# Performance work log

Hardware: AMD Instinct MI355X
Metric: run time of the kernel (lower is better)

## Reference

```python
import jax, jax.numpy as jnp
import numpy as np

B, S, DIM = 4, 2048, 1024


def _xavier(key, shape):
    # xavier_uniform for a [out, in] Linear weight
    fan_in, fan_out = shape[1], shape[0]
    limit = float(np.sqrt(6.0 / (fan_in + fan_out)))
    return jax.random.uniform(key, shape, jnp.float32, -limit, limit)


def setup_inputs() -> dict:
    key = jax.random.key(0)
    ks = jax.random.split(key, 8)
    z_real = jax.random.normal(ks[0], (B, S, DIM), jnp.float32)
    z_imag = jax.random.normal(ks[1], (B, S, DIM), jnp.float32)
    wq_r = _xavier(ks[2], (DIM, DIM))
    wq_i = _xavier(ks[3], (DIM, DIM))
    wk_r = _xavier(ks[4], (DIM, DIM))
    wk_i = _xavier(ks[5], (DIM, DIM))
    wv_r = _xavier(ks[6], (DIM, DIM))
    wv_i = _xavier(ks[7], (DIM, DIM))
    # causal mask (0 = masked), broadcast over batch
    mask = jnp.tril(jnp.ones((S, S), jnp.int32))
    return {"z_real": z_real, "z_imag": z_imag,
            "wq_r": wq_r, "wq_i": wq_i,
            "wk_r": wk_r, "wk_i": wk_i,
            "wv_r": wv_r, "wv_i": wv_i,
            "mask": mask}


def _complex_linear(xr, xi, wr, wi):
    # torch Linear: y = x @ W^T
    yr = xr @ wr.T - xi @ wi.T
    yi = xi @ wr.T + xr @ wi.T
    return yr, yi


def reference(z_real, z_imag, wq_r, wq_i, wk_r, wk_i, wv_r, wv_i, mask):
    dim = z_real.shape[-1]
    scale = dim ** (-0.5)
    qr, qi = _complex_linear(z_real, z_imag, wq_r, wq_i)
    kr, ki = _complex_linear(z_real, z_imag, wk_r, wk_i)
    vr, vi = _complex_linear(z_real, z_imag, wv_r, wv_i)
    # cat([q.real, q.imag]) @ cat([k.real, k.imag])^T == qr@kr^T + qi@ki^T
    scores = (jnp.einsum('bsd,btd->bst', qr, kr)
              + jnp.einsum('bsd,btd->bst', qi, ki)) * scale  # [B,S,S]
    scores = jnp.where(mask == 0, -jnp.inf, scores)
    attn = jax.nn.softmax(scores, axis=-1)
    out_r = jnp.einsum('bst,btd->bsd', attn, vr)
    out_i = jnp.einsum('bst,btd->bsd', attn, vi)
    return jnp.stack([out_r, out_i], axis=0)  # [2,B,S,dim] = (real, imag)
```

## Files before the change

kernel.cpp:

```cpp
#include <hip/hip_runtime.h>
#include <hip/hip_bf16.h>
#include <hip/hip_fp16.h>

#define DIMK 1024
#define SEQ  2048
#define BATCH 4
#define NTOK (BATCH*SEQ)
#define PROJ_ELEMS ((size_t)NTOK*DIMK)
#define LD 2048

typedef unsigned short ushort_t;
typedef __attribute__((ext_vector_type(8))) short short8;
typedef __attribute__((ext_vector_type(4))) float float4v;

#define MFMA_BF16 __builtin_amdgcn_mfma_f32_16x16x32_bf16

__device__ __forceinline__ unsigned short f2bf(float f) {
    union { float f; unsigned int i; } x; x.f = f;
    unsigned int r = x.i + 0x7fffu + ((x.i >> 16) & 1u);
    return (unsigned short)(r >> 16);
}

__device__ __forceinline__ void gld_lds16(const void* g, void* l) {
    auto gp = reinterpret_cast<const __attribute__((address_space(1))) unsigned int*>(
        reinterpret_cast<uintptr_t>(g));
    auto lp = reinterpret_cast<__attribute__((address_space(3))) unsigned int*>(
        reinterpret_cast<uintptr_t>(l));
    __builtin_amdgcn_global_load_lds(gp, lp, 16, 0, 0);
}

__device__ __forceinline__ void stage2(const ushort_t* __restrict__ gbase,
                                       ushort_t* lbase, int kcol,
                                       int rg0, int g, int scol)
{
    gld_lds16(gbase + (size_t)(rg0 * 16 + g) * LD + kcol + scol,
              lbase + rg0 * 512);
    gld_lds16(gbase + (size_t)(rg0 * 16 + 16 + g) * LD + kcol + scol,
              lbase + rg0 * 512 + 512);
}

__device__ __forceinline__ void gemm_core256(
    const ushort_t* __restrict__ Arow,
    const ushort_t* __restrict__ Brow,
    int kend,
    ushort_t* Alds, ushort_t* Blds,
    float4v acc[8][4], int wid, int lane)
{
    const int g    = lane >> 2;
    const int sx   = lane & 3;
    const int scol = ((sx - (g >> 1)) & 3) * 8;
    const int r16  = lane & 15;
    const int quad = lane >> 4;
    const int roff = r16 * 32 + ((quad + (r16 >> 1)) & 3) * 8;
    const int wm = wid >> 2, wn = wid & 3;
    const int rg0 = wid * 2;
    const int NT = kend >> 6;

    stage2(Brow, Blds,        0,  rg0, g, scol);
    stage2(Arow, Alds,        0,  rg0, g, scol);
    stage2(Brow, Blds + 8192, 32, rg0, g, scol);
    stage2(Arow, Alds + 8192, 32, rg0, g, scol);
    asm volatile("s_waitcnt vmcnt(4)" ::: "memory");
    __builtin_amdgcn_s_barrier();

    for (int t = 0; t < NT; ++t) {
        const int d     = (t & 1) << 14;
        const int dn    = d ^ 16384;
        const int knext = (t + 1) << 6;
        const bool pre  = (t + 1 < NT);
        short8 af[4], bf[4];

        #pragma unroll
        for (int j = 0; j < 4; ++j)
            bf[j] = *(const short8*)(Blds + d + (wn * 4 + j) * 512 + roff);
        #pragma unroll
        for (int ii = 0; ii < 4; ++ii)
            af[ii] = *(const short8*)(Alds + d + (wm * 8 + ii) * 512 + roff);
        if (pre) stage2(Brow, Blds + dn, knext, rg0, g, scol);
        asm volatile("" ::: "memory");
        __builtin_amdgcn_s_barrier();
        asm volatile("s_waitcnt lgkmcnt(0)" ::: "memory");
        __builtin_amdgcn_s_setprio(1);
        #pragma unroll
        for (int ii = 0; ii < 4; ++ii)
            #pragma unroll
            for (int j = 0; j < 4; ++j)
                acc[ii][j] = MFMA_BF16(af[ii], bf[j], acc[ii][j], 0, 0, 0);
        __builtin_amdgcn_s_setprio(0);
        asm volatile("" ::: "memory");
        __builtin_amdgcn_s_barrier();

        #pragma unroll
        for (int ii = 0; ii < 4; ++ii)
            af[ii] = *(const short8*)(Alds + d + (wm * 8 + 4 + ii) * 512 + roff);
        if (pre) {
            stage2(Arow, Alds + dn, knext, rg0, g, scol);
            asm volatile("s_waitcnt vmcnt(4)" ::: "memory");
        } else {
            asm volatile("s_waitcnt vmcnt(0)" ::: "memory");
        }
        __builtin_amdgcn_s_barrier();
        asm volatile("s_waitcnt lgkmcnt(0)" ::: "memory");
        __builtin_amdgcn_s_setprio(1);
        #pragma unroll
        for (int ii = 0; ii < 4; ++ii)
            #pragma unroll
            for (int j = 0; j < 4; ++j)
                acc[4 + ii][j] = MFMA_BF16(af[ii], bf[j], acc[4 + ii][j], 0, 0, 0);
        __builtin_amdgcn_s_setprio(0);
        asm volatile("" ::: "memory");
        __builtin_amdgcn_s_barrier();

        #pragma unroll
        for (int j = 0; j < 4; ++j)
            bf[j] = *(const short8*)(Blds + d + 8192 + (wn * 4 + j) * 512 + roff);
        #pragma unroll
        for (int ii = 0; ii < 4; ++ii)
            af[ii] = *(const short8*)(Alds + d + 8192 + (wm * 8 + ii) * 512 + roff);
        if (pre) stage2(Brow, Blds + dn + 8192, knext + 32, rg0, g, scol);
        asm volatile("" ::: "memory");
        __builtin_amdgcn_s_barrier();
        asm volatile("s_waitcnt lgkmcnt(0)" ::: "memory");
        __builtin_amdgcn_s_setprio(1);
        #pragma unroll
        for (int ii = 0; ii < 4; ++ii)
            #pragma unroll
            for (int j = 0; j < 4; ++j)
                acc[ii][j] = MFMA_BF16(af[ii], bf[j], acc[ii][j], 0, 0, 0);
        __builtin_amdgcn_s_setprio(0);
        asm volatile("" ::: "memory");
        __builtin_amdgcn_s_barrier();

        #pragma unroll
        for (int ii = 0; ii < 4; ++ii)
            af[ii] = *(const short8*)(Alds + d + 8192 + (wm * 8 + 4 + ii) * 512 + roff);
        if (pre) {
            stage2(Arow, Alds + dn + 8192, knext + 32, rg0, g, scol);
            asm volatile("s_waitcnt vmcnt(4)" ::: "memory");
        } else {
            asm volatile("" ::: "memory");
        }
        __builtin_amdgcn_s_barrier();
        asm volatile("s_waitcnt lgkmcnt(0)" ::: "memory");
        __builtin_amdgcn_s_setprio(1);
        #pragma unroll
        for (int ii = 0; ii < 4; ++ii)
            #pragma unroll
            for (int j = 0; j < 4; ++j)
                acc[4 + ii][j] = MFMA_BF16(af[ii], bf[j], acc[4 + ii][j], 0, 0, 0);
        __builtin_amdgcn_s_setprio(0);
        asm volatile("" ::: "memory");
        __builtin_amdgcn_s_barrier();
    }
}

__global__ __launch_bounds__(512, 2)
void gemm_proj(const ushort_t* __restrict__ A, const ushort_t* __restrict__ B,
               ushort_t* __restrict__ Cq, ushort_t* __restrict__ Ck,
               ushort_t* __restrict__ Cv)
{
    __shared__ ushort_t smem[65536];
    const int tid = threadIdx.x, wid = tid >> 6, lane = tid & 63;
    const int m0 = blockIdx.y * 256;
    const int n0g = blockIdx.x * 256;
    ushort_t* C = (n0g < 2048) ? Cq : ((n0g < 4096) ? Ck : Cv);
    const int n0 = n0g & 2047;
    float4v acc[8][4] = {};
    gemm_core256(A + (size_t)m0 * LD, B + (size_t)n0g * LD, 2048,
                 smem, smem + 32768, acc, wid, lane);

    const int wm = wid >> 2, wn = wid & 3;
    const int col16 = lane & 15, quad = lane >> 4;
    #pragma unroll
    for (int i = 0; i < 8; ++i)
        #pragma unroll
        for (int j = 0; j < 4; ++j) {
            const int n = n0 + wn * 64 + j * 16 + col16;
            #pragma unroll
            for (int r = 0; r < 4; ++r) {
                const int m = m0 + wm * 128 + i * 16 + quad * 4 + r;
                C[(size_t)m * LD + n] = f2bf(acc[i][j][r]);
            }
        }
}

__global__ __launch_bounds__(512, 2)
void gemm_scores(const ushort_t* __restrict__ Q, const ushort_t* __restrict__ K,
                 __half* __restrict__ S)
{
    const int jt = blockIdx.x, it = blockIdx.y, b = blockIdx.z;
    if (jt > it) return;
    __shared__ ushort_t smem[65536];
    const int tid = threadIdx.x, wid = tid >> 6, lane = tid & 63;
    const size_t boff = (size_t)b * SEQ * LD;
    float4v acc[8][4] = {};
    gemm_core256(Q + boff + (size_t)it * 256 * LD, K + boff + (size_t)jt * 256 * LD,
                 2048, smem, smem + 32768, acc, wid, lane);

    const int wm = wid >> 2, wn = wid & 3;
    const int col16 = lane & 15, quad = lane >> 4;
    const float scale = 0.03125f;
    __half* Sb = S + (size_t)b * SEQ * SEQ;
    #pragma unroll
    for (int i = 0; i < 8; ++i)
        #pragma unroll
        for (int j = 0; j < 4; ++j) {
            const int t = jt * 256 + wn * 64 + j * 16 + col16;
            #pragma unroll
            for (int r = 0; r < 4; ++r) {
                const int s = it * 256 + wm * 128 + i * 16 + quad * 4 + r;
                Sb[(size_t)s * SEQ + t] = __float2half(acc[i][j][r] * scale);
            }
        }
}

__global__ __launch_bounds__(512, 2)
void gemm_pv(const ushort_t* __restrict__ P, const ushort_t* __restrict__ VT,
             float* __restrict__ out)
{
    const int nt = blockIdx.x, mt = blockIdx.y, b = blockIdx.z;
    __shared__ ushort_t smem[65536];
    const int tid = threadIdx.x, wid = tid >> 6, lane = tid & 63;
    const int kend = (mt + 1) * 256;
    float4v acc[8][4] = {};
    gemm_core256(P + (size_t)b * SEQ * SEQ + (size_t)mt * 256 * LD,
                 VT + (size_t)b * LD * LD + (size_t)nt * 256 * LD,
                 kend, smem, smem + 32768, acc, wid, lane);

    const int wm = wid >> 2, wn = wid & 3;
    const int col16 = lane & 15, quad = lane >> 4;
    #pragma unroll
    for (int i = 0; i < 8; ++i)
        #pragma unroll
        for (int j = 0; j < 4; ++j) {
            const int n = nt * 256 + wn * 64 + j * 16 + col16;
            float* dst = out + ((n < 1024) ? 0 : PROJ_ELEMS);
            const int d = n & 1023;
            #pragma unroll
            for (int r = 0; r < 4; ++r) {
                const int s = mt * 256 + wm * 128 + i * 16 + quad * 4 + r;
                dst[((size_t)b * SEQ + s) * DIMK + d] = acc[i][j][r];
            }
        }
}

__global__ __launch_bounds__(256)
void zcat_kernel(const float* __restrict__ zr, const float* __restrict__ zi,
                 ushort_t* __restrict__ zcat)
{
    const size_t e = ((size_t)blockIdx.x * 256 + threadIdx.x) * 8;
    const size_t tok = e >> 11;
    const int c = (int)(e & 2047);
    const float* src = (c < 1024) ? (zr + tok * 1024 + c) : (zi + tok * 1024 + (c - 1024));
    float4 a = *(const float4*)src;
    float4 b = *(const float4*)(src + 4);
    ushort_t* d = zcat + e;
    d[0]=f2bf(a.x); d[1]=f2bf(a.y); d[2]=f2bf(a.z); d[3]=f2bf(a.w);
    d[4]=f2bf(b.x); d[5]=f2bf(b.y); d[6]=f2bf(b.z); d[7]=f2bf(b.w);
}

__global__ __launch_bounds__(256)
void wstack_kernel(const float* __restrict__ wr, const float* __restrict__ wi,
                   ushort_t* __restrict__ ws)
{
    const size_t e = ((size_t)blockIdx.x * 256 + threadIdx.x) * 8;
    const int n = (int)(e >> 11), c = (int)(e & 2047);
    const int n1 = n & 1023, c1 = c & 1023;
    const float* src;
    float sgn = 1.f;
    if (n < 1024) {
        if (c < 1024) src = wr + (size_t)n1 * 1024 + c1;
        else        { src = wi + (size_t)n1 * 1024 + c1; sgn = -1.f; }
    } else {
        src = ((c < 1024) ? wi : wr) + (size_t)n1 * 1024 + c1;
    }
    float4 a = *(const float4*)src;
    float4 b = *(const float4*)(src + 4);
    ushort_t* d = ws + e;
    d[0]=f2bf(sgn*a.x); d[1]=f2bf(sgn*a.y); d[2]=f2bf(sgn*a.z); d[3]=f2bf(sgn*a.w);
    d[4]=f2bf(sgn*b.x); d[5]=f2bf(sgn*b.y); d[6]=f2bf(sgn*b.z); d[7]=f2bf(sgn*b.w);
}

__global__ __launch_bounds__(256)
void transpose_v(const ushort_t* __restrict__ vcat, ushort_t* __restrict__ vt)
{
    __shared__ ushort_t tile[64][65];
    const int b = blockIdx.z;
    const int t0 = blockIdx.x * 64, c0 = blockIdx.y * 64;
    const int tid = threadIdx.x;
    const int r = tid >> 4, c4 = (tid & 15) * 4;
    const ushort_t* src = vcat + ((size_t)(b * SEQ + t0)) * LD + c0;
    #pragma unroll
    for (int p = 0; p < 4; ++p) {
        const int row = p * 16 + r;
        ushort4 v = *(const ushort4*)(src + (size_t)row * LD + c4);
        tile[row][c4+0]=v.x; tile[row][c4+1]=v.y; tile[row][c4+2]=v.z; tile[row][c4+3]=v.w;
    }
    __syncthreads();
    ushort_t* dst = vt + ((size_t)b * LD + c0) * LD + t0;
    #pragma unroll
    for (int p = 0; p < 4; ++p) {
        const int crow = p * 16 + r;
        ushort4 v;
        v.x = tile[c4+0][crow]; v.y = tile[c4+1][crow];
        v.z = tile[c4+2][crow]; v.w = tile[c4+3][crow];
        *(ushort4*)(dst + (size_t)crow * LD + c4) = v;
    }
}

__global__ __launch_bounds__(256)
void softmax_kernel(__half* __restrict__ sc)
{
    const int row = blockIdx.x;
    const int s = row & (SEQ - 1);
    __half* x = sc + (size_t)row * SEQ;
    ushort_t* xo = (ushort_t*)x;
    const int n = s + 1;
    const int tid = threadIdx.x, wave = tid >> 6, lane = tid & 63;
    __shared__ float redm[4], reds[4];

    float m = -1e30f;
    for (int i = tid; i < n; i += 256) m = fmaxf(m, __half2float(x[i]));
    #pragma unroll
    for (int off = 32; off > 0; off >>= 1) m = fmaxf(m, __shfl_down(m, off, 64));
    if (lane == 0) redm[wave] = m;
    __syncthreads();
    if (tid == 0) redm[0] = fmaxf(fmaxf(redm[0], redm[1]), fmaxf(redm[2], redm[3]));
    __syncthreads();
    m = redm[0];

    float l = 0.f;
    for (int i = tid; i < n; i += 256) l += __expf(__half2float(x[i]) - m);
    #pragma unroll
    for (int off = 32; off > 0; off >>= 1) l += __shfl_down(l, off, 64);
    if (lane == 0) reds[wave] = l;
    __syncthreads();
    if (tid == 0) reds[0] = reds[0] + reds[1] + reds[2] + reds[3];
    __syncthreads();
    const float inv = 1.0f / reds[0];

    const int npad = min(SEQ, ((s >> 8) + 1) << 8);
    for (int i = tid; i < npad; i += 256) {
        float v = (i < n) ? __expf(__half2float(x[i]) - m) * inv : 0.f;
        xo[i] = f2bf(v);
    }
}

extern "C" void kernel_launch(void* const* d_in, const int* in_sizes, int n_in,
                              void* d_out, int out_size, void* d_ws, size_t ws_size,
                              hipStream_t stream)
{
    const float* z_real = (const float*)d_in[0];
    const float* z_imag = (const float*)d_in[1];
    const float* wq_r   = (const float*)d_in[2];
    const float* wq_i   = (const float*)d_in[3];
    const float* wk_r   = (const float*)d_in[4];
    const float* wk_i   = (const float*)d_in[5];
    const float* wv_r   = (const float*)d_in[6];
    const float* wv_i   = (const float*)d_in[7];

    uint8_t* ws = (uint8_t*)d_ws;
    ushort_t* zcat = (ushort_t*)(ws + 0);
    ushort_t* wall = (ushort_t*)(ws + 33554432);
    ushort_t* wsq  = wall;
    ushort_t* wsk  = (ushort_t*)(ws + 33554432 + 8388608);
    ushort_t* wsv  = (ushort_t*)(ws + 33554432 + 16777216);
    ushort_t* qcat = (ushort_t*)(ws + 58720256);
    ushort_t* kcat = (ushort_t*)(ws + 92274688);
    ushort_t* vcat = (ushort_t*)(ws + 125829120);
    ushort_t* vt   = (ushort_t*)(ws + 0);
    __half*   sc   = (__half*)(ws + 125829120);
    float*    outp = (float*)d_out;

    zcat_kernel<<<dim3(8192), dim3(256), 0, stream>>>(z_real, z_imag, zcat);
    wstack_kernel<<<dim3(2048), dim3(256), 0, stream>>>(wq_r, wq_i, wsq);
    wstack_kernel<<<dim3(2048), dim3(256), 0, stream>>>(wk_r, wk_i, wsk);
    wstack_kernel<<<dim3(2048), dim3(256), 0, stream>>>(wv_r, wv_i, wsv);

    gemm_proj<<<dim3(24, 32), dim3(512), 0, stream>>>(zcat, wall, qcat, kcat, vcat);

    transpose_v<<<dim3(32, 32, 4), dim3(256), 0, stream>>>(vcat, vt);
    gemm_scores<<<dim3(8, 8, 4), dim3(512), 0, stream>>>(qcat, kcat, sc);
    softmax_kernel<<<dim3(NTOK), dim3(256), 0, stream>>>(sc);
    gemm_pv<<<dim3(8, 8, 4), dim3(512), 0, stream>>>((ushort_t*)sc, vt, outp);
}
```

Before: 491.3 us.

## Double-buffer MFMA register fragments to overlap LDS reads with compute

Restructures the GEMM main loop so each phase reads the next fragment set from LDS into a second register buffer while MFMAs run on the previously loaded one. The explicit lgkmcnt(0) waits before each MFMA block are removed. Global-to-LDS staging of A and B is now issued together, with the vmcnt waits moved after compute. This hides LDS latency behind matrix math at the cost of more live VGPRs. It also risks subtle ordering hazards around the shared buffers.

```diff
diff --git a/kernel.cpp b/kernel.cpp
--- a/kernel.cpp
+++ b/kernel.cpp
@@ -52,9 +52,12 @@
     const int r16  = lane & 15;
     const int quad = lane >> 4;
     const int roff = r16 * 32 + ((quad + (r16 >> 1)) & 3) * 8;
-    const int wm = wid >> 2, wn = wid & 3;
+    const int wm8 = (wid >> 2) * 8;
+    const int wn4 = (wid & 3) * 4;
     const int rg0 = wid * 2;
     const int NT = kend >> 6;
+
+    short8 a0[4], b0[4], a1[4], b1[4];
 
     stage2(Brow, Blds,        0,  rg0, g, scol);
     stage2(Arow, Alds,        0,  rg0, g, scol);
@@ -62,92 +65,98 @@
     stage2(Arow, Alds + 8192, 32, rg0, g, scol);
     asm volatile("s_waitcnt vmcnt(4)" ::: "memory");
     __builtin_amdgcn_s_barrier();
+    #pragma unroll
+    for (int j = 0; j < 4; ++j)
+        b0[j] = *(const short8*)(Blds + (wn4 + j) * 512 + roff);
+    #pragma unroll
+    for (int i = 0; i < 4; ++i)
+        a0[i] = *(const short8*)(Alds + (wm8 + i) * 512 + roff);
 
     for (int t = 0; t < NT; ++t) {
         const int d     = (t & 1) << 14;
         const int dn    = d ^ 16384;
         const int knext = (t + 1) << 6;
         const bool pre  = (t + 1 < NT);
-        short8 af[4], bf[4];
 
         #pragma unroll
         for (int j = 0; j < 4; ++j)
-            bf[j] = *(const short8*)(Blds + d + (wn * 4 + j) * 512 + roff);
-        #pragma unroll
-        for (int ii = 0; ii < 4; ++ii)
-            af[ii] = *(const short8*)(Alds + d + (wm * 8 + ii) * 512 + roff);
-        if (pre) stage2(Brow, Blds + dn, knext, rg0, g, scol);
-        asm volatile("" ::: "memory");
-        __builtin_amdgcn_s_barrier();
-        asm volatile("s_waitcnt lgkmcnt(0)" ::: "memory");
+            b1[j] = *(const short8*)(Blds + d + (wn4 + j) * 512 + roff);
+        #pragma unroll
+        for (int i = 0; i < 4; ++i)
+            a1[i] = *(const short8*)(Alds + d + (wm8 + 4 + i) * 512 + roff);
+        if (pre) {
+            stage2(Brow, Blds + dn, knext, rg0, g, scol);
+            stage2(Arow, Alds + dn, knext, rg0, g, scol);
+        }
+        asm volatile("" ::: "memory");
+        __builtin_amdgcn_s_barrier();
         __builtin_amdgcn_s_setprio(1);
         #pragma unroll
-        for (int ii = 0; ii < 4; ++ii)
-            #pragma unroll
-            for (int j = 0; j < 4; ++j)
-                acc[ii][j] = MFMA_BF16(af[ii], bf[j], acc[ii][j], 0, 0, 0);
+        for (int i = 0; i < 4; ++i)
+            #pragma unroll
+            for (int j = 0; j < 4; ++j)
+                acc[i][j] = MFMA_BF16(a0[i], b0[j], acc[i][j], 0, 0, 0);
         __builtin_amdgcn_s_setprio(0);
-        asm volatile("" ::: "memory");
-        __builtin_amdgcn_s_barrier();
-
-        #pragma unroll
-        for (int ii = 0; ii < 4; ++ii)
-            af[ii] = *(const short8*)(Alds + d + (wm * 8 + 4 + ii) * 512 + roff);
+        if (pre) asm volatile("s_waitcnt vmcnt(4)" ::: "memory");
+        else     asm volatile("s_waitcnt vmcnt(0)" ::: "memory");
+        __builtin_amdgcn_s_barrier();
+
+        #pragma unroll
+        for (int j = 0; j < 4; ++j)
+            b0[j] = *(const short8*)(Blds + d + 8192 + (wn4 + j) * 512 + roff);
+        #pragma unroll
+        for (int i = 0; i < 4; ++i)
+            a0[i] = *(const short8*)(Alds + d + 8192 + (wm8 + i) * 512 + roff);
         if (pre) {
-            stage2(Arow, Alds + dn, knext, rg0, g, scol);
-            asm volatile("s_waitcnt vmcnt(4)" ::: "memory");
-        } else {
-            asm volatile("s_waitcnt vmcnt(0)" ::: "memory");
-        }
-        __builtin_amdgcn_s_barrier();
-        asm volatile("s_waitcnt lgkmcnt(0)" ::: "memory");
+            stage2(Brow, Blds + dn + 8192, knext + 32, rg0, g, scol);
+            stage2(Arow, Alds + dn + 8192, knext + 32, rg0, g, scol);
+        }
+        asm volatile("" ::: "memory");
+        __builtin_amdgcn_s_barrier();
         __builtin_amdgcn_s_setprio(1);
         #pragma unroll
-        for (int ii = 0; ii < 4; ++ii)
-            #pragma unroll
-            for (int j = 0; j < 4; ++j)
-                acc[4 + ii][j] = MFMA_BF16(af[ii], bf[j], acc[4 + ii][j], 0, 0, 0);
+        for (int i = 0; i < 4; ++i)
+            #pragma unroll
+            for (int j = 0; j < 4; ++j)
+                acc[4 + i][j] = MFMA_BF16(a1[i], b1[j], acc[4 + i][j], 0, 0, 0);
         __builtin_amdgcn_s_setprio(0);
         asm volatile("" ::: "memory");
         __builtin_amdgcn_s_barrier();
 
         #pragma unroll
         for (int j = 0; j < 4; ++j)
-            bf[j] = *(const short8*)(Blds + d + 8192 + (wn * 4 + j) * 512 + roff);
-        #pragma unroll
-        for (int ii = 0; ii < 4; ++ii)
-            af[ii] = *(const short8*)(Alds + d + 8192 + (wm * 8 + ii) * 512 + roff);
-        if (pre) stage2(Brow, Blds + dn + 8192, knext + 32, rg0, g, scol);
-        asm volatile("" ::: "memory");
-        __builtin_amdgcn_s_barrier();
-        asm volatile("s_waitcnt lgkmcnt(0)" ::: "memory");
+            b1[j] = *(const short8*)(Blds + d + 8192 + (wn4 + j) * 512 + roff);
+        #pragma unroll
+        for (int i = 0; i < 4; ++i)
+            a1[i] = *(const short8*)(Alds + d + 8192 + (wm8 + 4 + i) * 512 + roff);
+        asm volatile("" ::: "memory");
+        __builtin_amdgcn_s_barrier();
         __builtin_amdgcn_s_setprio(1);
         #pragma unroll
-        for (int ii = 0; ii < 4; ++ii)
-            #pragma unroll
-            for (int j = 0; j < 4; ++j)
-                acc[ii][j] = MFMA_BF16(af[ii], bf[j], acc[ii][j], 0, 0, 0);
+        for (int i = 0; i < 4; ++i)
+            #pragma unroll
+            for (int j = 0; j < 4; ++j)
+                acc[i][j] = MFMA_BF16(a0[i], b0[j], acc[i][j], 0, 0, 0);
         __builtin_amdgcn_s_setprio(0);
-        asm volatile("" ::: "memory");
-        __builtin_amdgcn_s_barrier();
-
-        #pragma unroll
-        for (int ii = 0; ii < 4; ++ii)
-            af[ii] = *(const short8*)(Alds + d + 8192 + (wm * 8 + 4 + ii) * 512 + roff);
+        if (pre) asm volatile("s_waitcnt vmcnt(4)" ::: "memory");
+        __builtin_amdgcn_s_barrier();
+
         if (pre) {
-            stage2(Arow, Alds + dn + 8192, knext + 32, rg0, g, scol);
-            asm volatile("s_waitcnt vmcnt(4)" ::: "memory");
-        } else {
-            asm volatile("" ::: "memory");
-        }
-        __builtin_amdgcn_s_barrier();
-        asm volatile("s_waitcnt lgkmcnt(0)" ::: "memory");
+            #pragma unroll
+            for (int j = 0; j < 4; ++j)
+                b0[j] = *(const short8*)(Blds + dn + (wn4 + j) * 512 + roff);
+            #pragma unroll
+            for (int i = 0; i < 4; ++i)
+                a0[i] = *(const short8*)(Alds + dn + (wm8 + i) * 512 + roff);
+        }
+        asm volatile("" ::: "memory");
+        __builtin_amdgcn_s_barrier();
         __builtin_amdgcn_s_setprio(1);
         #pragma unroll
-        for (int ii = 0; ii < 4; ++ii)
-            #pragma unroll
-            for (int j = 0; j < 4; ++j)
-                acc[4 + ii][j] = MFMA_BF16(af[ii], bf[j], acc[4 + ii][j], 0, 0, 0);
+        for (int i = 0; i < 4; ++i)
+            #pragma unroll
+            for (int j = 0; j < 4; ++j)
+                acc[4 + i][j] = MFMA_BF16(a1[i], b1[j], acc[4 + i][j], 0, 0, 0);
         __builtin_amdgcn_s_setprio(0);
         asm volatile("" ::: "memory");
         __builtin_amdgcn_s_barrier();
```

Result: slower. 518.9 us (+5.6%).
